# Optimization experiments

Measured on AMD Instinct MI355X. Metric: run time of the kernel, lower is better.

Reference implementation:

```python
import math
import jax, jax.numpy as jnp
import numpy as np

B, C, D = 4, 1024, 2048
N_EXP, TOP_K, CAP_F = 8, 2, 1.25


def setup_inputs() -> dict:
    key = jax.random.key(0)
    k1, k2, k3, k4 = jax.random.split(key, 4)
    x = jax.random.normal(k1, (B, C, D), dtype=jnp.float32)
    noise = jax.random.normal(k2, (B, C, N_EXP), dtype=jnp.float32)
    w_g = jax.random.normal(k3, (N_EXP, D), dtype=jnp.float32) * 0.02
    w_noise = jax.random.normal(k4, (N_EXP, D), dtype=jnp.float32) * 0.02
    return {"x": x, "noise": noise, "w_g": w_g, "w_noise": w_noise}


def reference(x, noise, w_g, w_noise):
    b, c, d = x.shape
    T = b * c  # num_tokens
    E, k = w_g.shape[0], TOP_K

    # gating logits with noisy top-k (noise eps passed in explicitly)
    logits = jnp.einsum('bcd,ed->bce', x, w_g)
    logits = logits + jax.nn.softplus(jnp.einsum('bcd,ed->bce', x, w_noise)) * noise

    top_vals, top_idx = jax.lax.top_k(logits, k)  # (B,C,k)

    # scatter top-k logits into -inf tensor then softmax == mask non-topk to -inf
    onehot_k = jax.nn.one_hot(top_idx, E, dtype=jnp.int32)  # (B,C,k,E)
    topk_mask = onehot_k.sum(axis=-2) > 0                   # (B,C,E)
    router_probs = jax.nn.softmax(jnp.where(topk_mask, logits, -jnp.inf), axis=-1)

    cap = math.floor(k * CAP_F * T / E)
    cap += cap % 2

    # (k, T, E) expert assignment mask
    exp_mask = onehot_k.reshape(T, k, E).transpose(1, 0, 2)
    # position-in-expert rank via cumulative sum over (k*T, E)
    exp_rank = jnp.cumsum(exp_mask.reshape(k * T, E), axis=0) - 1
    exp_rank = exp_rank.reshape(k, T, E)
    exp_mask = exp_mask * (exp_rank < cap).astype(jnp.int32)
    rank = jnp.sum(exp_mask * exp_rank, axis=-1)  # (k, T) int

    probs_flat = router_probs.reshape(T, E)[None]          # (1,T,E)
    w = exp_mask.astype(x.dtype) * probs_flat              # (k,T,E)
    rank_oh = jax.nn.one_hot(rank, cap, dtype=x.dtype)     # (k,T,cap)
    # combine weights: (T, E, cap)
    exp_weights = jnp.einsum('kte,ktc->tec', w, rank_oh)
    exp_mask_out = exp_weights != 0                        # bool (T,E,cap)

    x_flat = x.reshape(T, d)
    # dense one-hot dispatch matmul: (E, cap, T) @ (T, d)
    expert_batches = jnp.einsum('tec,td->ecd', exp_mask_out.astype(x.dtype), x_flat)
    return exp_weights, exp_mask_out, expert_batches
```

## Files before the change

kernel.cpp:

```cpp
#include <hip/hip_runtime.h>

#define T_TOKENS 4096
#define D_DIM    2048
#define NEXP     8
#define CAP      1280
#define NSLOTS   (NEXP * CAP)

#define K1_BLOCKS 1024
#define FILL_FLOATS (2ull * T_TOKENS * NSLOTS)
#define FILL_VECS   (FILL_FLOATS / 4)
#define FILL_THREADS (K1_BLOCKS * 256)

typedef float f32x4 __attribute__((ext_vector_type(4)));

__global__ void gate_fill_kernel(const float* __restrict__ x,
                                 const float* __restrict__ noise,
                                 const float* __restrict__ w_g,
                                 const float* __restrict__ w_noise,
                                 int*   __restrict__ top_idx,
                                 float* __restrict__ top_prob,
                                 float* __restrict__ wm_base)
{
    const int wave = threadIdx.x >> 6;
    const int lane = threadIdx.x & 63;
    const int t = blockIdx.x * 4 + wave;

    const f32x4* xv = reinterpret_cast<const f32x4*>(x + (size_t)t * D_DIM);

    float acc[16];
#pragma unroll
    for (int j = 0; j < 16; ++j) acc[j] = 0.f;

#pragma unroll
    for (int it = 0; it < 8; ++it) {
        const int c = it * 64 + lane;
        const f32x4 xval = xv[c];
#pragma unroll
        for (int e = 0; e < NEXP; ++e) {
            const f32x4 g = reinterpret_cast<const f32x4*>(w_g + (size_t)e * D_DIM)[c];
            acc[e] += xval.x * g.x + xval.y * g.y + xval.z * g.z + xval.w * g.w;
            const f32x4 n = reinterpret_cast<const f32x4*>(w_noise + (size_t)e * D_DIM)[c];
            acc[8 + e] += xval.x * n.x + xval.y * n.y + xval.z * n.z + xval.w * n.w;
        }
    }

#pragma unroll
    for (int j = 0; j < 16; ++j) {
        float v = acc[j];
#pragma unroll
        for (int off = 32; off > 0; off >>= 1) v += __shfl_down(v, off, 64);
        acc[j] = v;
    }

    if (lane == 0) {
        float logit[NEXP];
#pragma unroll
        for (int e = 0; e < NEXP; ++e) {
            const float z = acc[8 + e];
            const float sp = fmaxf(z, 0.f) + log1pf(expf(-fabsf(z)));
            logit[e] = acc[e] + sp * noise[(size_t)t * NEXP + e];
        }
        int i0 = 0; float v0 = logit[0];
#pragma unroll
        for (int e = 1; e < NEXP; ++e) {
            if (logit[e] > v0) { v0 = logit[e]; i0 = e; }
        }
        int i1 = -1; float v1 = -3.402823466e38f;
#pragma unroll
        for (int e = 0; e < NEXP; ++e) {
            if (e != i0 && logit[e] > v1) { v1 = logit[e]; i1 = e; }
        }
        const float e1  = expf(v1 - v0);
        const float inv = 1.f / (1.f + e1);
        top_idx[t]            = i0;
        top_idx[T_TOKENS + t] = i1;
        top_prob[t]            = inv;
        top_prob[T_TOKENS + t] = e1 * inv;
    }

    const size_t tid = (size_t)blockIdx.x * 256 + threadIdx.x;
    f32x4* dst = reinterpret_cast<f32x4*>(wm_base);
    const f32x4 z = {0.f, 0.f, 0.f, 0.f};
#pragma unroll
    for (int j = 0; j < (int)(FILL_VECS / FILL_THREADS); ++j)
        dst[(size_t)j * FILL_THREADS + tid] = z;
}

__global__ void scan_scatter_kernel(const int*   __restrict__ top_idx,
                                    const float* __restrict__ top_prob,
                                    int*   __restrict__ slot_token,
                                    float* __restrict__ exp_weights,
                                    float* __restrict__ exp_mask)
{
    __shared__ int sidx[2 * T_TOKENS];
    __shared__ int scnt[8];

    const int e    = blockIdx.x;
    const int w    = threadIdx.x >> 6;
    const int lane = threadIdx.x & 63;

    for (int i = threadIdx.x; i < 2 * T_TOKENS; i += 512)
        sidx[i] = top_idx[i];
    for (int r = threadIdx.x; r < CAP; r += 512)
        slot_token[e * CAP + r] = -1;
    __syncthreads();

    int cnt = 0;
#pragma unroll
    for (int c = 0; c < 16; ++c) {
        const int i = (w * 16 + c) * 64 + lane;
        cnt += __popcll(__ballot(sidx[i] == e));
    }
    if (lane == 0) scnt[w] = cnt;
    __syncthreads();

    int base = 0;
#pragma unroll
    for (int j = 0; j < 8; ++j) if (j < w) base += scnt[j];

#pragma unroll
    for (int c = 0; c < 16; ++c) {
        const int i = (w * 16 + c) * 64 + lane;
        const bool match = (sidx[i] == e);
        const unsigned long long m = __ballot(match);
        if (match) {
            const int r = base + __popcll(m & ((1ull << lane) - 1ull));
            if (r < CAP) {
                slot_token[e * CAP + r] = i;
                const int t = i & (T_TOKENS - 1);
                const float wgt = top_prob[i];
                const size_t off = (size_t)t * NSLOTS + e * CAP + r;
                exp_weights[off] = wgt;
                exp_mask[off]    = (wgt != 0.f) ? 1.f : 0.f;
            }
        }
        base += __popcll(m);
    }
}

__global__ void batches_kernel(const float* __restrict__ x,
                               const int*   __restrict__ slot_token,
                               float* __restrict__ expert_batches)
{
    const int slot = blockIdx.x;
    const int i = slot_token[slot];
    f32x4* dst = reinterpret_cast<f32x4*>(expert_batches + (size_t)slot * D_DIM);

    if (i >= 0) {
        const int t = i & (T_TOKENS - 1);
        const f32x4* src = reinterpret_cast<const f32x4*>(x + (size_t)t * D_DIM);
#pragma unroll
        for (int c = threadIdx.x; c < D_DIM / 4; c += 256)
            dst[c] = src[c];
    } else {
        const f32x4 z = {0.f, 0.f, 0.f, 0.f};
#pragma unroll
        for (int c = threadIdx.x; c < D_DIM / 4; c += 256)
            dst[c] = z;
    }
}

extern "C" void kernel_launch(void* const* d_in, const int* in_sizes, int n_in,
                              void* d_out, int out_size, void* d_ws, size_t ws_size,
                              hipStream_t stream)
{
    const float* x       = (const float*)d_in[0];
    const float* noise   = (const float*)d_in[1];
    const float* w_g     = (const float*)d_in[2];
    const float* w_noise = (const float*)d_in[3];

    float* out = (float*)d_out;
    const size_t n_ew = (size_t)T_TOKENS * NEXP * CAP;
    float* exp_weights    = out;
    float* exp_mask       = out + n_ew;
    float* expert_batches = out + 2 * n_ew;

    int*   top_idx    = (int*)d_ws;
    float* top_prob   = (float*)((char*)d_ws + 2 * T_TOKENS * 4);
    int*   slot_token = (int*)((char*)d_ws + 4 * T_TOKENS * 4);

    gate_fill_kernel<<<K1_BLOCKS, 256, 0, stream>>>(
        x, noise, w_g, w_noise, top_idx, top_prob, exp_weights);
    scan_scatter_kernel<<<NEXP, 512, 0, stream>>>(top_idx, top_prob, slot_token,
                                                  exp_weights, exp_mask);
    batches_kernel<<<NSLOTS, 256, 0, stream>>>(x, slot_token, expert_batches);
}
```

Measured before the change: 128.2 us.

## Split zero-fill into hipMemset and stage gate weights in LDS, two tokens per wave

The zero-fill of the exp_weights and exp_mask outputs moves out of the fused gating kernel into a hipMemsetAsync. The gating kernel now stages w_g and w_noise chunks in shared memory and has each wave compute two tokens, so weight loads are reused across 16 tokens per block. This removes redundant global weight reads but serializes the fill with gating instead of overlapping them inside one kernel. It also adds block-level syncs.

```diff
diff --git a/kernel.cpp b/kernel.cpp
--- a/kernel.cpp
+++ b/kernel.cpp
@@ -6,84 +6,112 @@
 #define CAP      1280
 #define NSLOTS   (NEXP * CAP)
 
-#define K1_BLOCKS 1024
-#define FILL_FLOATS (2ull * T_TOKENS * NSLOTS)
-#define FILL_VECS   (FILL_FLOATS / 4)
-#define FILL_THREADS (K1_BLOCKS * 256)
+#define GATE_TPB   512
+#define GATE_TPW   2
+#define GATE_TPBK  16
+#define GATE_BLOCKS (T_TOKENS / GATE_TPBK)
+#define GCHUNK     512
+#define GCHUNK4    (GCHUNK / 4)
+#define NCHUNK     (D_DIM / GCHUNK)
 
 typedef float f32x4 __attribute__((ext_vector_type(4)));
 
-__global__ void gate_fill_kernel(const float* __restrict__ x,
-                                 const float* __restrict__ noise,
-                                 const float* __restrict__ w_g,
-                                 const float* __restrict__ w_noise,
-                                 int*   __restrict__ top_idx,
-                                 float* __restrict__ top_prob,
-                                 float* __restrict__ wm_base)
-{
-    const int wave = threadIdx.x >> 6;
+__device__ __forceinline__ float dot4(f32x4 a, f32x4 b) {
+    return a.x * b.x + a.y * b.y + a.z * b.z + a.w * b.w;
+}
+
+__global__ void gating_kernel(const float* __restrict__ x,
+                              const float* __restrict__ noise,
+                              const float* __restrict__ w_g,
+                              const float* __restrict__ w_noise,
+                              int*   __restrict__ top_idx,
+                              float* __restrict__ top_prob)
+{
+    __shared__ f32x4 s_wg[NEXP][GCHUNK4];
+    __shared__ f32x4 s_wn[NEXP][GCHUNK4];
+
+    const int w    = threadIdx.x >> 6;
     const int lane = threadIdx.x & 63;
-    const int t = blockIdx.x * 4 + wave;
-
-    const f32x4* xv = reinterpret_cast<const f32x4*>(x + (size_t)t * D_DIM);
-
-    float acc[16];
-#pragma unroll
-    for (int j = 0; j < 16; ++j) acc[j] = 0.f;
-
-#pragma unroll
-    for (int it = 0; it < 8; ++it) {
-        const int c = it * 64 + lane;
-        const f32x4 xval = xv[c];
+    const int t0   = blockIdx.x * GATE_TPBK + w * GATE_TPW;
+
+    const f32x4* x0 = reinterpret_cast<const f32x4*>(x + (size_t)t0 * D_DIM);
+    const f32x4* x1 = reinterpret_cast<const f32x4*>(x + (size_t)(t0 + 1) * D_DIM);
+
+    float accg[GATE_TPW][NEXP];
+    float accn[GATE_TPW][NEXP];
+#pragma unroll
+    for (int τ = 0; τ < GATE_TPW; ++τ)
+#pragma unroll
+        for (int e = 0; e < NEXP; ++e) { accg[τ][e] = 0.f; accn[τ][e] = 0.f; }
+
+    for (int ch = 0; ch < NCHUNK; ++ch) {
+        const int base4 = ch * GCHUNK4;
+#pragma unroll
+        for (int j = threadIdx.x; j < NEXP * GCHUNK4; j += GATE_TPB) {
+            const int e = j / GCHUNK4, c = j % GCHUNK4;
+            s_wg[e][c] = reinterpret_cast<const f32x4*>(w_g     + (size_t)e * D_DIM)[base4 + c];
+            s_wn[e][c] = reinterpret_cast<const f32x4*>(w_noise + (size_t)e * D_DIM)[base4 + c];
+        }
+        __syncthreads();
+
+#pragma unroll
+        for (int i = 0; i < GCHUNK4 / 64; ++i) {
+            const int c = i * 64 + lane;
+            const f32x4 xv0 = x0[base4 + c];
+            const f32x4 xv1 = x1[base4 + c];
+#pragma unroll
+            for (int e = 0; e < NEXP; ++e) {
+                const f32x4 g = s_wg[e][c];
+                const f32x4 n = s_wn[e][c];
+                accg[0][e] += dot4(xv0, g);
+                accg[1][e] += dot4(xv1, g);
+                accn[0][e] += dot4(xv0, n);
+                accn[1][e] += dot4(xv1, n);
+            }
+        }
+        __syncthreads();
+    }
+
+#pragma unroll
+    for (int τ = 0; τ < GATE_TPW; ++τ)
 #pragma unroll
         for (int e = 0; e < NEXP; ++e) {
-            const f32x4 g = reinterpret_cast<const f32x4*>(w_g + (size_t)e * D_DIM)[c];
-            acc[e] += xval.x * g.x + xval.y * g.y + xval.z * g.z + xval.w * g.w;
-            const f32x4 n = reinterpret_cast<const f32x4*>(w_noise + (size_t)e * D_DIM)[c];
-            acc[8 + e] += xval.x * n.x + xval.y * n.y + xval.z * n.z + xval.w * n.w;
-        }
-    }
-
-#pragma unroll
-    for (int j = 0; j < 16; ++j) {
-        float v = acc[j];
-#pragma unroll
-        for (int off = 32; off > 0; off >>= 1) v += __shfl_down(v, off, 64);
-        acc[j] = v;
-    }
+            float vg = accg[τ][e], vn = accn[τ][e];
+#pragma unroll
+            for (int off = 32; off > 0; off >>= 1) {
+                vg += __shfl_down(vg, off, 64);
+                vn += __shfl_down(vn, off, 64);
+            }
+            accg[τ][e] = vg; accn[τ][e] = vn;
+        }
 
     if (lane == 0) {
-        float logit[NEXP];
-#pragma unroll
-        for (int e = 0; e < NEXP; ++e) {
-            const float z = acc[8 + e];
-            const float sp = fmaxf(z, 0.f) + log1pf(expf(-fabsf(z)));
-            logit[e] = acc[e] + sp * noise[(size_t)t * NEXP + e];
-        }
-        int i0 = 0; float v0 = logit[0];
-#pragma unroll
-        for (int e = 1; e < NEXP; ++e) {
-            if (logit[e] > v0) { v0 = logit[e]; i0 = e; }
-        }
-        int i1 = -1; float v1 = -3.402823466e38f;
-#pragma unroll
-        for (int e = 0; e < NEXP; ++e) {
-            if (e != i0 && logit[e] > v1) { v1 = logit[e]; i1 = e; }
-        }
-        const float e1  = expf(v1 - v0);
-        const float inv = 1.f / (1.f + e1);
-        top_idx[t]            = i0;
-        top_idx[T_TOKENS + t] = i1;
-        top_prob[t]            = inv;
-        top_prob[T_TOKENS + t] = e1 * inv;
-    }
-
-    const size_t tid = (size_t)blockIdx.x * 256 + threadIdx.x;
-    f32x4* dst = reinterpret_cast<f32x4*>(wm_base);
-    const f32x4 z = {0.f, 0.f, 0.f, 0.f};
-#pragma unroll
-    for (int j = 0; j < (int)(FILL_VECS / FILL_THREADS); ++j)
-        dst[(size_t)j * FILL_THREADS + tid] = z;
+#pragma unroll
+        for (int τ = 0; τ < GATE_TPW; ++τ) {
+            const int t = t0 + τ;
+            float logit[NEXP];
+#pragma unroll
+            for (int e = 0; e < NEXP; ++e) {
+                const float z = accn[τ][e];
+                const float sp = fmaxf(z, 0.f) + log1pf(expf(-fabsf(z)));
+                logit[e] = accg[τ][e] + sp * noise[(size_t)t * NEXP + e];
+            }
+            int i0 = 0; float v0 = logit[0];
+#pragma unroll
+            for (int e = 1; e < NEXP; ++e)
+                if (logit[e] > v0) { v0 = logit[e]; i0 = e; }
+            int i1 = -1; float v1 = -3.402823466e38f;
+#pragma unroll
+            for (int e = 0; e < NEXP; ++e)
+                if (e != i0 && logit[e] > v1) { v1 = logit[e]; i1 = e; }
+            const float e1  = expf(v1 - v0);
+            const float inv = 1.f / (1.f + e1);
+            top_idx[t]            = i0;
+            top_idx[T_TOKENS + t] = i1;
+            top_prob[t]            = inv;
+            top_prob[T_TOKENS + t] = e1 * inv;
+        }
+    }
 }
 
 __global__ void scan_scatter_kernel(const int*   __restrict__ top_idx,
@@ -179,8 +207,10 @@
     float* top_prob   = (float*)((char*)d_ws + 2 * T_TOKENS * 4);
     int*   slot_token = (int*)((char*)d_ws + 4 * T_TOKENS * 4);
 
-    gate_fill_kernel<<<K1_BLOCKS, 256, 0, stream>>>(
-        x, noise, w_g, w_noise, top_idx, top_prob, exp_weights);
+    (void)hipMemsetAsync(out, 0, 2 * n_ew * sizeof(float), stream);
+
+    gating_kernel<<<GATE_BLOCKS, GATE_TPB, 0, stream>>>(x, noise, w_g, w_noise,
+                                                        top_idx, top_prob);
     scan_scatter_kernel<<<NEXP, 512, 0, stream>>>(top_idx, top_prob, slot_token,
                                                   exp_weights, exp_mask);
     batches_kernel<<<NSLOTS, 256, 0, stream>>>(x, slot_token, expert_batches);
```

Result: slower. 135.3 us (+5.6%).
